# Performance work log

Hardware: AMD Instinct MI355X
Metric: run time of the kernel (lower is better)

Reference implementation:

```python
import jax, jax.numpy as jnp
import numpy as np


def _aggregate(xyz, node, features, k):
    # xyz: [B,3,N], node: [B,3,M], features: [B,C,N] -> [B,C,M]
    # squared euclidean distances via expansion (same math as (x-n)^2 sum)
    d = (jnp.sum(xyz ** 2, axis=1)[:, :, None]
         + jnp.sum(node ** 2, axis=1)[:, None, :]
         - 2.0 * jnp.einsum('bdn,bdm->bnm', xyz, node))  # [B,N,M]
    # k smallest over N for each of M nodes (order irrelevant: max-pool after)
    _, nn_idx = jax.lax.top_k(-jnp.transpose(d, (0, 2, 1)), k)  # [B,M,k]
    # gather C-channel features at neighbor indices -> [B,C,M,k]
    g = jnp.take_along_axis(features[:, :, None, :], nn_idx[:, None, :, :], axis=3)
    return jnp.max(g, axis=3)  # [B,C,M]


def setup_inputs() -> dict:
    key = jax.random.key(0)
    k1, k2, k3, k4 = jax.random.split(key, 4)
    B, N, C = 4, 16384, 128
    return {
        'input_coords': jax.random.normal(k1, (B, 3, N), dtype=jnp.float32),
        'input_feats': jax.random.normal(k2, (B, C, N), dtype=jnp.float32),
        'W': jax.random.normal(k3, (C, C), dtype=jnp.float32) * 0.05,
        'b': jax.random.normal(k4, (C,), dtype=jnp.float32) * 0.05,
        'num_sample': 2048,
        'num_agg': 16,
    }


def reference(input_coords, input_feats, W, b, num_sample, num_agg):
    # Dropout in eval mode -> identity. proj = 1x1 Conv1d == per-point linear.
    Z = input_feats  # [B,C,N]
    proj = jax.nn.relu(jnp.einsum('oc,bcn->bon', W, Z) + b[None, :, None])
    vector = jnp.max(proj, axis=-1, keepdims=True)  # [B,C,1]
    weights = jnp.sum(input_feats * vector, axis=1)  # [B,N]
    scores = jax.nn.sigmoid(weights)
    values, idx = jax.lax.top_k(scores, num_sample)  # [B,M] each, sorted desc
    pool_coords_static = jnp.take_along_axis(input_coords, idx[:, None, :], axis=2)  # [B,3,M]
    pool_feats_static = jnp.take_along_axis(input_feats, idx[:, None, :], axis=2)    # [B,C,M]
    v = values[:, None, :]  # [B,1,M]
    pool_feats = pool_feats_static * v
    pool_coords = pool_coords_static * v
    agg_feats = _aggregate(input_coords, pool_coords_static, input_feats, num_agg)  # [B,C,M]
    pool_feats = jnp.concatenate([pool_feats, agg_feats], axis=1)  # [B,2C,M]
    return (pool_coords_static, pool_coords, pool_feats)
```

## Files before the change

kernel.cpp:

```cpp
#include <hip/hip_runtime.h>
#include <hip/hip_bf16.h>
#include <stdint.h>

#define BB 4
#define NN 16384
#define CC 128
#define MM 2048
#define KNN 16
#define QCAPG 512
#define EPS 1e-3f

typedef unsigned int u32;
typedef unsigned short u16;
typedef unsigned long long u64;

#define OFF_FEATT   0ull
#define OFF_PTS4    33554432ull
#define OFF_WT      37748736ull
#define OFF_KEYS    37814272ull
#define OFF_VEC     38338560ull
#define OFF_IDX     38340608ull
#define OFF_VAL     38373376ull
#define OFF_TMP1    38406144ull
#define OFF_TMP2    38668288ull
#define OFF_QCNT    38799360ull
#define OFF_Q       38832128ull

__device__ __forceinline__ float np_dist(float4 p, float4 nd) {
#pragma clang fp contract(off)
    float dot = ((p.x * nd.x) + (p.y * nd.y)) + (p.z * nd.z);
    float d = (p.w + nd.w) - 2.0f * dot;
    return d;
}

__device__ __forceinline__ float sfast(float4 p, float4 nd) {
    float dot = fmaf(p.x, nd.x, fmaf(p.y, nd.y, p.z * nd.z));
    return fmaf(-2.0f, dot, p.w);
}

__device__ __forceinline__ u32 mono_bits(float d) {
    u32 u = __float_as_uint(d);
    u ^= ((u32)(((int)u) >> 31)) | 0x80000000u;
    return u;
}

__device__ __forceinline__ float kth16(float v, int l) {
    float sv = v;
#pragma unroll
    for (int k = 2; k <= 64; k <<= 1) {
#pragma unroll
        for (int j = k >> 1; j > 0; j >>= 1) {
            float pv = __shfl_xor(sv, j);
            bool up = ((l & k) == 0);
            bool tmin = (((l & j) == 0) == up);
            float mn = fminf(sv, pv), mx = fmaxf(sv, pv);
            sv = tmin ? mn : mx;
        }
    }
    return __shfl(sv, 15);
}

__global__ void k_prep(const float* __restrict__ coords, const float* __restrict__ W,
                       float4* __restrict__ pts4, float* __restrict__ WT,
                       u32* __restrict__ vecU, u32* __restrict__ qcnt) {
    int g = blockIdx.x * 256 + threadIdx.x;
    if (g < BB * NN) {
        int b = g >> 14, n = g & (NN - 1);
        const float* cb = coords + (size_t)b * 3 * NN;
        float x = cb[n], y = cb[NN + n], z = cb[2 * NN + n];
        float w;
        {
#pragma clang fp contract(off)
            w = ((x * x) + (y * y)) + (z * z);
        }
        pts4[g] = make_float4(x, y, z, w);
    } else if (g < BB * NN + CC * CC) {
        int i = g - BB * NN;
        int o = i >> 7, c = i & 127;
        WT[c * CC + o] = W[i];
    } else if (g < BB * NN + CC * CC + BB * CC) {
        vecU[g - BB * NN - CC * CC] = 0u;
    } else if (g < BB * NN + CC * CC + BB * CC + BB * MM) {
        qcnt[g - BB * NN - CC * CC - BB * CC] = 0u;
    }
}

__global__ void k_transpose(const float* __restrict__ feats, float* __restrict__ feat_t) {
    __shared__ float t[64][65];
    int bx = blockIdx.x;
    int b = bx >> 9; int rem = bx & 511; int nb = rem >> 1; int cb2 = rem & 1;
    int n0 = nb * 64, c0 = cb2 * 64;
    int l = threadIdx.x & 63, r0 = threadIdx.x >> 6;
    const float* fb = feats + (size_t)b * CC * NN;
#pragma unroll
    for (int p = 0; p < 16; ++p) {
        int r = r0 + p * 4;
        t[r][l] = fb[(size_t)(c0 + r) * NN + n0 + l];
    }
    __syncthreads();
    float* ob = feat_t + (size_t)b * NN * CC;
#pragma unroll
    for (int p = 0; p < 16; ++p) {
        int r = r0 + p * 4;
        ob[(size_t)(n0 + r) * CC + c0 + l] = t[l][r];
    }
}

__global__ __launch_bounds__(256, 4) void k_vec(const float* __restrict__ feats,
        const float* __restrict__ WT, const float* __restrict__ bias, u32* __restrict__ vecU) {
    __shared__ float Wl[CC * 64];
    int bx = blockIdx.x;
    int oh = bx & 1;
    int ntile = (bx >> 1) & 63;
    int b = bx >> 7;
    int n0 = ntile * 256;
    int tid = threadIdx.x, l = tid & 63;
    int w = __builtin_amdgcn_readfirstlane(tid >> 6);
    for (int i = tid; i < CC * 64; i += 256) {
        int c = i >> 6, op = i & 63;
        Wl[i] = WT[c * CC + oh * 64 + op];
    }
    __syncthreads();
    int o0 = w * 16;
    const float* zb = feats + (size_t)b * CC * NN + n0 + 4 * l;
    float bo[16];
#pragma unroll
    for (int oi = 0; oi < 16; ++oi) bo[oi] = bias[oh * 64 + o0 + oi];
    float acc0[16], acc1[16], acc2[16], acc3[16];
#pragma unroll
    for (int oi = 0; oi < 16; ++oi) { acc0[oi] = bo[oi]; acc1[oi] = bo[oi]; acc2[oi] = bo[oi]; acc3[oi] = bo[oi]; }
    float4 zpre = *(const float4*)zb;
#pragma unroll 2
    for (int c = 0; c < CC; ++c) {
        float4 z = zpre;
        if (c + 1 < CC) zpre = *(const float4*)(zb + (size_t)(c + 1) * NN);
        const float* wr = Wl + c * 64 + o0;
        float4 w0 = *(const float4*)(wr);
        float4 w1 = *(const float4*)(wr + 4);
        float4 w2 = *(const float4*)(wr + 8);
        float4 w3 = *(const float4*)(wr + 12);
        float wv[16] = {w0.x, w0.y, w0.z, w0.w, w1.x, w1.y, w1.z, w1.w,
                        w2.x, w2.y, w2.z, w2.w, w3.x, w3.y, w3.z, w3.w};
#pragma unroll
        for (int oi = 0; oi < 16; ++oi) {
            acc0[oi] = fmaf(wv[oi], z.x, acc0[oi]);
            acc1[oi] = fmaf(wv[oi], z.y, acc1[oi]);
            acc2[oi] = fmaf(wv[oi], z.z, acc2[oi]);
            acc3[oi] = fmaf(wv[oi], z.w, acc3[oi]);
        }
    }
#pragma unroll
    for (int oi = 0; oi < 16; ++oi) {
        float r0 = acc0[oi] > 0.0f ? acc0[oi] : 0.0f;
        float r1 = acc1[oi] > 0.0f ? acc1[oi] : 0.0f;
        float r2 = acc2[oi] > 0.0f ? acc2[oi] : 0.0f;
        float r3 = acc3[oi] > 0.0f ? acc3[oi] : 0.0f;
        float rv = fmaxf(fmaxf(r0, r1), fmaxf(r2, r3));
#pragma unroll
        for (int s = 32; s; s >>= 1) rv = fmaxf(rv, __shfl_xor(rv, s));
        if (l == 0) atomicMax(vecU + b * CC + oh * 64 + o0 + oi, __float_as_uint(rv));
    }
}

__global__ void k_scores(const float* __restrict__ feats, const float* __restrict__ vecF,
                         u64* __restrict__ keys) {
    int i = blockIdx.x * 256 + threadIdx.x;
    int b = i >> 14, n = i & (NN - 1);
    const float* fb = feats + (size_t)b * CC * NN + n;
    const float* vb = vecF + b * CC;
    float wsum = 0.f;
#pragma unroll 8
    for (int c = 0; c < CC; ++c) wsum = fmaf(fb[(size_t)c * NN], vb[c], wsum);
    float s = 1.0f / (1.0f + expf(-wsum));
    u32 mono = __float_as_uint(s);
    keys[i] = ((u64)mono << 32) | (u64)(0xFFFFFFFFu - (u32)n);
}

__global__ __launch_bounds__(1024) void k_sortchunk(u64* __restrict__ keys) {
    __shared__ u64 sk[2048];
    int b = blockIdx.x >> 3, c = blockIdx.x & 7;
    int tid = threadIdx.x;
    u64* src = keys + (size_t)b * NN + c * 2048;
    sk[tid] = src[tid];
    sk[tid + 1024] = src[tid + 1024];
    for (int size = 2; size <= 2048; size <<= 1) {
        for (int stride = size >> 1; stride > 0; stride >>= 1) {
            __syncthreads();
            int t = tid;
            int i = (t << 1) - (t & (stride - 1));
            int j = i + stride;
            u64 a = sk[i], cc = sk[j];
            bool up = ((i & size) == 0);
            if ((a < cc) == up) { sk[i] = cc; sk[j] = a; }
        }
    }
    __syncthreads();
    src[tid] = sk[tid];
    src[tid + 1024] = sk[tid + 1024];
}

__global__ __launch_bounds__(512) void k_mergetop(const u64* __restrict__ in,
        u64* __restrict__ outp, int lg ) {
    __shared__ u64 mk[4096];
    int b = blockIdx.x >> lg, pr = blockIdx.x & ((1 << lg) - 1);
    int tid = threadIdx.x;
    const u64* s0 = in + ((size_t)((b << lg) + pr) * 2) * 2048;
    const u64* s1 = s0 + 2048;
    for (int t = tid; t < 2048; t += 512) { mk[t] = s0[t]; mk[2048 + t] = s1[2047 - t]; }
    __syncthreads();
    for (int t = tid; t < 2048; t += 512) {
        u64 a = mk[t], c = mk[t + 2048];
        if (a < c) { mk[t] = c; mk[t + 2048] = a; }
    }
    for (int stride = 1024; stride > 0; stride >>= 1) {
        __syncthreads();
        for (int t = tid; t < 1024; t += 512) {
            int i = (t << 1) - (t & (stride - 1));
            int j = i + stride;
            u64 a = mk[i], c = mk[j];
            if (a < c) { mk[i] = c; mk[j] = a; }
        }
    }
    __syncthreads();
    u64* dst = outp + (size_t)((b << lg) + pr) * 2048;
    for (int t = tid; t < 2048; t += 512) dst[t] = mk[t];
}

__global__ __launch_bounds__(512) void k_mergefinal(const u64* __restrict__ in,
        u32* __restrict__ idxA, float* __restrict__ valA) {
    __shared__ u64 mk[4096];
    int b = blockIdx.x, tid = threadIdx.x;
    const u64* s0 = in + (size_t)(b * 2) * 2048;
    const u64* s1 = s0 + 2048;
    for (int t = tid; t < 2048; t += 512) { mk[t] = s0[t]; mk[2048 + t] = s1[2047 - t]; }
    __syncthreads();
    for (int t = tid; t < 2048; t += 512) {
        u64 a = mk[t], c = mk[t + 2048];
        if (a < c) { mk[t] = c; mk[t + 2048] = a; }
    }
    for (int stride = 1024; stride > 0; stride >>= 1) {
        __syncthreads();
        for (int t = tid; t < 1024; t += 512) {
            int i = (t << 1) - (t & (stride - 1));
            int j = i + stride;
            u64 a = mk[i], c = mk[j];
            if (a < c) { mk[i] = c; mk[j] = a; }
        }
    }
    __syncthreads();
    for (int t = tid; t < 2048; t += 512) {
        u64 k = mk[t];
        idxA[b * MM + t] = 0xFFFFFFFFu - (u32)(k & 0xFFFFFFFFull);
        valA[b * MM + t] = __uint_as_float((u32)(k >> 32));
    }
}

__global__ void k_gather(const float4* __restrict__ pts4, const float* __restrict__ feat_t,
        const u32* __restrict__ idxA, const float* __restrict__ valA, float* __restrict__ out) {
    int g = blockIdx.x * 256 + threadIdx.x;
    int b = g >> 11, i = g & (MM - 1);
    u32 n = idxA[g];
    float v = valA[g];
    float4 p = pts4[(b << 14) + (int)n];
    float* o0 = out + (size_t)b * 3 * MM + i;
    o0[0] = p.x; o0[MM] = p.y; o0[2 * MM] = p.z;
    float* o1 = o0 + 24576;
    o1[0] = p.x * v; o1[MM] = p.y * v; o1[2 * MM] = p.z * v;
    const float4* ft = (const float4*)(feat_t + ((size_t)(b << 14) + n) * CC);
    float* o2 = out + 49152 + ((size_t)b * 256) * MM + i;
#pragma unroll 8
    for (int q = 0; q < 32; ++q) {
        float4 f = ft[q];
        o2[(size_t)(4 * q + 0) * MM] = f.x * v;
        o2[(size_t)(4 * q + 1) * MM] = f.y * v;
        o2[(size_t)(4 * q + 2) * MM] = f.z * v;
        o2[(size_t)(4 * q + 3) * MM] = f.w * v;
    }
}

__device__ __forceinline__ void emit_q(u32* __restrict__ qcnt, u32* __restrict__ q,
        int gn, u64 bal, bool pred, int n, int l) {
    int cnt = (int)__popcll(bal);
    u32 base = 0;
    if (l == 0) base = atomicAdd(qcnt + gn, (u32)cnt);
    base = (u32)__shfl((int)base, 0);
    if (pred) {
        int off = (int)__popcll(bal & ((1ull << l) - 1ull));
        u32 slot = base + (u32)off;
        if (slot < QCAPG) q[(size_t)gn * QCAPG + slot] = (u32)n;
    }
}

__global__ __launch_bounds__(256) void k_knnS(const float4* __restrict__ pts4,
        const u32* __restrict__ idxA, u32* __restrict__ qcnt, u32* __restrict__ q) {
    __shared__ float4 ptsS[1024];
    __shared__ float4 nodeS[8];
    int bx = blockIdx.x;
    int b = bx >> 9;
    int idx = bx & 511;
    int ng = idx >> 1;
    int half = idx & 1;
    int tid = threadIdx.x, l = tid & 63;
    int w = __builtin_amdgcn_readfirstlane(tid >> 6);
    const float4* pb = pts4 + (b << 14);
    if (tid < 8) nodeS[tid] = pb[idxA[b * MM + ng * 8 + tid]];
#pragma unroll
    for (int j = 0; j < 4; ++j) ptsS[tid + 256 * j] = pb[tid + 256 * j];
    __syncthreads();
    float4 nd0 = nodeS[w * 2 + 0];
    float4 nd1 = nodeS[w * 2 + 1];
    float lm0 = 3.0e38f, lm1 = 3.0e38f;
#pragma unroll 4
    for (int j = 0; j < 16; ++j) {
        float4 p = ptsS[l + 64 * j];
        lm0 = fminf(lm0, sfast(p, nd0));
        lm1 = fminf(lm1, sfast(p, nd1));
    }
    __syncthreads();
#pragma unroll
    for (int j = 0; j < 4; ++j) ptsS[tid + 256 * j] = pb[1024 + tid + 256 * j];
    __syncthreads();
#pragma unroll 4
    for (int j = 0; j < 16; ++j) {
        float4 p = ptsS[l + 64 * j];
        lm0 = fminf(lm0, sfast(p, nd0));
        lm1 = fminf(lm1, sfast(p, nd1));
    }
    float T0 = kth16(lm0, l) + 2.0f * EPS;
    float T1 = kth16(lm1, l) + 2.0f * EPS;
    int gn0 = (b << 11) + ng * 8 + w * 2;
    for (int ch = half * 8; ch < half * 8 + 8; ++ch) {
        __syncthreads();
#pragma unroll
        for (int j = 0; j < 4; ++j) ptsS[tid + 256 * j] = pb[ch * 1024 + tid + 256 * j];
        __syncthreads();
        for (int j = 0; j < 16; ++j) {
            float4 p = ptsS[l + 64 * j];
            int n = ch * 1024 + l + 64 * j;
            float dt0 = fmaf(p.x, nd0.x, fmaf(p.y, nd0.y, p.z * nd0.z));
            float s0 = fmaf(-2.0f, dt0, p.w);
            float dt1 = fmaf(p.x, nd1.x, fmaf(p.y, nd1.y, p.z * nd1.z));
            float s1 = fmaf(-2.0f, dt1, p.w);
            bool p0 = (s0 <= T0);
            bool p1 = (s1 <= T1);
            u64 bal0 = __ballot(p0);
            if (bal0) emit_q(qcnt, q, gn0, bal0, p0, n, l);
            u64 bal1 = __ballot(p1);
            if (bal1) emit_q(qcnt, q, gn0 + 1, bal1, p1, n, l);
        }
    }
}

__global__ __launch_bounds__(256) void k_knnM(const float4* __restrict__ pts4,
        const float* __restrict__ feat_t, const u32* __restrict__ idxA,
        const u32* __restrict__ qcnt, const u32* __restrict__ q, float* __restrict__ out) {
    int w = __builtin_amdgcn_readfirstlane(threadIdx.x >> 6);
    int g = blockIdx.x * 4 + w;
    int b = g >> 11, m = g & (MM - 1);
    int l = threadIdx.x & 63;
    const float4* pb = pts4 + (b << 14);
    float4 nd = pb[idxA[g]];
    int cnt = (int)qcnt[g];
    if (cnt > QCAPG) cnt = QCAPG;
    const u32* qq = q + (size_t)g * QCAPG;
    u64 regk[QCAPG / 64];
#pragma unroll
    for (int s = 0; s < QCAPG / 64; ++s) {
        u64 kk = ~0ull;
        if ((s << 6) < cnt) {
            int pos = (s << 6) + l;
            if (pos < cnt) {
                u32 n = qq[pos];
                float d = np_dist(pb[n], nd);
                kk = ((u64)mono_bits(d) << 32) | (u64)n;
            }
        }
        regk[s] = kk;
    }
    float mx0 = -3.0e38f, mx1 = -3.0e38f;
    for (int it = 0; it < KNN; ++it) {
        u64 mykey = ~0ull;
#pragma unroll
        for (int s = 0; s < QCAPG / 64; ++s)
            if ((s << 6) < cnt) mykey = regk[s] < mykey ? regk[s] : mykey;
        u64 r = mykey;
#pragma unroll
        for (int j = 32; j > 0; j >>= 1) {
            u64 o = __shfl_xor(r, j);
            r = o < r ? o : r;
        }
#pragma unroll
        for (int s = 0; s < QCAPG / 64; ++s)
            if ((s << 6) < cnt) { if (regk[s] == r) regk[s] = ~0ull; }
        if (r != ~0ull) {
            u32 nj = (u32)(r & 0xFFFFFFFFull);
            const float2 f = *(const float2*)(feat_t + ((size_t)(b << 14) + nj) * CC + (l << 1));
            mx0 = fmaxf(mx0, f.x);
            mx1 = fmaxf(mx1, f.y);
        }
    }
    size_t ob = 49152 + ((size_t)(b * 256 + 128 + 2 * l)) * MM + m;
    out[ob] = mx0;
    out[ob + MM] = mx1;
}

extern "C" void kernel_launch(void* const* d_in, const int* in_sizes, int n_in,
                              void* d_out, int out_size, void* d_ws, size_t ws_size,
                              hipStream_t stream) {
    const float* coords = (const float*)d_in[0];
    const float* feats  = (const float*)d_in[1];
    const float* W      = (const float*)d_in[2];
    const float* bias   = (const float*)d_in[3];
    char* ws = (char*)d_ws;
    float*  feat_t = (float*)(ws + OFF_FEATT);
    float4* pts4   = (float4*)(ws + OFF_PTS4);
    float*  WT     = (float*)(ws + OFF_WT);
    u64*    keys   = (u64*)(ws + OFF_KEYS);
    u32*    vecU   = (u32*)(ws + OFF_VEC);
    u32*    idxA   = (u32*)(ws + OFF_IDX);
    float*  valA   = (float*)(ws + OFF_VAL);
    u64*    tmp1   = (u64*)(ws + OFF_TMP1);
    u64*    tmp2   = (u64*)(ws + OFF_TMP2);
    u32*    qcnt   = (u32*)(ws + OFF_QCNT);
    u32*    q      = (u32*)(ws + OFF_Q);
    float*  out    = (float*)d_out;

    int prepN = BB * NN + CC * CC + BB * CC + BB * MM;
    k_prep     <<<(prepN + 255) / 256, 256, 0, stream>>>(coords, W, pts4, WT, vecU, qcnt);
    k_vec      <<<512, 256, 0, stream>>>(feats, WT, bias, vecU);
    k_transpose<<<BB * (NN / 64) * (CC / 64), 256, 0, stream>>>(feats, feat_t);
    k_scores   <<<BB * NN / 256, 256, 0, stream>>>(feats, (const float*)vecU, keys);
    k_sortchunk<<<BB * 8, 1024, 0, stream>>>(keys);
    k_mergetop <<<BB * 4, 512, 0, stream>>>(keys, tmp1, 2);
    k_mergetop <<<BB * 2, 512, 0, stream>>>(tmp1, tmp2, 1);
    k_mergefinal<<<BB, 512, 0, stream>>>(tmp2, idxA, valA);
    k_gather   <<<BB * MM / 256, 256, 0, stream>>>(pts4, feat_t, idxA, valA, out);
    k_knnS     <<<2048, 256, 0, stream>>>(pts4, idxA, qcnt, q);
    k_knnM     <<<BB * MM / 4, 256, 0, stream>>>(pts4, feat_t, idxA, qcnt, q, out);
}
```

Measured before the change: 277.0 us.

## Split KNN threshold into separate kernel and transpose candidate scan to point-major tiles

Moves the per-node k-th distance threshold estimate, taken from the first 2048 points, into its own kernel that writes a threshold array. The scan kernel now gives each thread one point and loops over 256 nodes held in shared memory, with each node's threshold packed into the w component. Before, each wave kept two nodes in registers and streamed points through shared memory. The change removes the duplicated threshold work that both halves of the old split repeated and cuts shared-memory traffic and barriers. In exchange it adds a kernel launch and gives up the dual-node interleaving. The ballot, atomic and emit logic now runs once per node per wave, which may serialize on atomics.

```diff
diff --git a/kernel.cpp b/kernel.cpp
--- a/kernel.cpp
+++ b/kernel.cpp
@@ -25,6 +25,7 @@
 #define OFF_TMP2    38668288ull
 #define OFF_QCNT    38799360ull
 #define OFF_Q       38832128ull
+#define OFF_T       55609344ull
 
 __device__ __forceinline__ float np_dist(float4 p, float4 nd) {
 #pragma clang fp contract(off)
@@ -278,75 +279,58 @@
     }
 }
 
-__device__ __forceinline__ void emit_q(u32* __restrict__ qcnt, u32* __restrict__ q,
-        int gn, u64 bal, bool pred, int n, int l) {
-    int cnt = (int)__popcll(bal);
-    u32 base = 0;
-    if (l == 0) base = atomicAdd(qcnt + gn, (u32)cnt);
-    base = (u32)__shfl((int)base, 0);
-    if (pred) {
-        int off = (int)__popcll(bal & ((1ull << l) - 1ull));
-        u32 slot = base + (u32)off;
-        if (slot < QCAPG) q[(size_t)gn * QCAPG + slot] = (u32)n;
-    }
+__global__ __launch_bounds__(256) void k_knnT(const float4* __restrict__ pts4,
+        const u32* __restrict__ idxA, float* __restrict__ Tarr) {
+    int w = __builtin_amdgcn_readfirstlane(threadIdx.x >> 6);
+    int g = blockIdx.x * 4 + w;
+    int b = g >> 11;
+    int l = threadIdx.x & 63;
+    const float4* pb = pts4 + (b << 14);
+    float4 nd = pb[idxA[g]];
+    float lm = 3.0e38f;
+#pragma unroll 8
+    for (int j = 0; j < 32; ++j) lm = fminf(lm, sfast(pb[l + 64 * j], nd));
+    float T16 = kth16(lm, l);
+    if (l == 0) Tarr[g] = T16 + 2.0f * EPS;
 }
 
 __global__ __launch_bounds__(256) void k_knnS(const float4* __restrict__ pts4,
-        const u32* __restrict__ idxA, u32* __restrict__ qcnt, u32* __restrict__ q) {
-    __shared__ float4 ptsS[1024];
-    __shared__ float4 nodeS[8];
+        const u32* __restrict__ idxA, const float* __restrict__ Tarr,
+        u32* __restrict__ qcnt, u32* __restrict__ q) {
+    __shared__ float4 nodeS[256];
     int bx = blockIdx.x;
     int b = bx >> 9;
-    int idx = bx & 511;
-    int ng = idx >> 1;
-    int half = idx & 1;
+    int rem = bx & 511;
+    int tile = rem >> 3;
+    int nc = rem & 7;
     int tid = threadIdx.x, l = tid & 63;
     int w = __builtin_amdgcn_readfirstlane(tid >> 6);
     const float4* pb = pts4 + (b << 14);
-    if (tid < 8) nodeS[tid] = pb[idxA[b * MM + ng * 8 + tid]];
-#pragma unroll
-    for (int j = 0; j < 4; ++j) ptsS[tid + 256 * j] = pb[tid + 256 * j];
-    __syncthreads();
-    float4 nd0 = nodeS[w * 2 + 0];
-    float4 nd1 = nodeS[w * 2 + 1];
-    float lm0 = 3.0e38f, lm1 = 3.0e38f;
+    int gnb = (b << 11) + nc * 256;
+    {
+        float4 nd = pb[idxA[gnb + tid]];
+        nodeS[tid] = make_float4(nd.x, nd.y, nd.z, Tarr[gnb + tid]);
+    }
+    __syncthreads();
+    int n = tile * 256 + w * 64 + l;
+    float4 p = pb[n];
 #pragma unroll 4
-    for (int j = 0; j < 16; ++j) {
-        float4 p = ptsS[l + 64 * j];
-        lm0 = fminf(lm0, sfast(p, nd0));
-        lm1 = fminf(lm1, sfast(p, nd1));
-    }
-    __syncthreads();
-#pragma unroll
-    for (int j = 0; j < 4; ++j) ptsS[tid + 256 * j] = pb[1024 + tid + 256 * j];
-    __syncthreads();
-#pragma unroll 4
-    for (int j = 0; j < 16; ++j) {
-        float4 p = ptsS[l + 64 * j];
-        lm0 = fminf(lm0, sfast(p, nd0));
-        lm1 = fminf(lm1, sfast(p, nd1));
-    }
-    float T0 = kth16(lm0, l) + 2.0f * EPS;
-    float T1 = kth16(lm1, l) + 2.0f * EPS;
-    int gn0 = (b << 11) + ng * 8 + w * 2;
-    for (int ch = half * 8; ch < half * 8 + 8; ++ch) {
-        __syncthreads();
-#pragma unroll
-        for (int j = 0; j < 4; ++j) ptsS[tid + 256 * j] = pb[ch * 1024 + tid + 256 * j];
-        __syncthreads();
-        for (int j = 0; j < 16; ++j) {
-            float4 p = ptsS[l + 64 * j];
-            int n = ch * 1024 + l + 64 * j;
-            float dt0 = fmaf(p.x, nd0.x, fmaf(p.y, nd0.y, p.z * nd0.z));
-            float s0 = fmaf(-2.0f, dt0, p.w);
-            float dt1 = fmaf(p.x, nd1.x, fmaf(p.y, nd1.y, p.z * nd1.z));
-            float s1 = fmaf(-2.0f, dt1, p.w);
-            bool p0 = (s0 <= T0);
-            bool p1 = (s1 <= T1);
-            u64 bal0 = __ballot(p0);
-            if (bal0) emit_q(qcnt, q, gn0, bal0, p0, n, l);
-            u64 bal1 = __ballot(p1);
-            if (bal1) emit_q(qcnt, q, gn0 + 1, bal1, p1, n, l);
+    for (int k = 0; k < 256; ++k) {
+        float4 nt = nodeS[k];
+        float dt = fmaf(p.x, nt.x, fmaf(p.y, nt.y, p.z * nt.z));
+        float s = fmaf(-2.0f, dt, p.w);
+        bool pred = (s <= nt.w);
+        u64 bal = __ballot(pred);
+        if (bal) {
+            int cnt = (int)__popcll(bal);
+            u32 base = 0;
+            if (l == 0) base = atomicAdd(qcnt + gnb + k, (u32)cnt);
+            base = (u32)__shfl((int)base, 0);
+            if (pred) {
+                int off = (int)__popcll(bal & ((1ull << l) - 1ull));
+                u32 slot = base + (u32)off;
+                if (slot < QCAPG) q[(size_t)(gnb + k) * QCAPG + slot] = (u32)n;
+            }
         }
     }
 }
@@ -423,6 +407,7 @@
     u64*    tmp2   = (u64*)(ws + OFF_TMP2);
     u32*    qcnt   = (u32*)(ws + OFF_QCNT);
     u32*    q      = (u32*)(ws + OFF_Q);
+    float*  Tarr   = (float*)(ws + OFF_T);
     float*  out    = (float*)d_out;
 
     int prepN = BB * NN + CC * CC + BB * CC + BB * MM;
@@ -435,6 +420,7 @@
     k_mergetop <<<BB * 2, 512, 0, stream>>>(tmp1, tmp2, 1);
     k_mergefinal<<<BB, 512, 0, stream>>>(tmp2, idxA, valA);
     k_gather   <<<BB * MM / 256, 256, 0, stream>>>(pts4, feat_t, idxA, valA, out);
-    k_knnS     <<<2048, 256, 0, stream>>>(pts4, idxA, qcnt, q);
+    k_knnT     <<<BB * MM / 4, 256, 0, stream>>>(pts4, idxA, Tarr);
+    k_knnS     <<<2048, 256, 0, stream>>>(pts4, idxA, Tarr, qcnt, q);
     k_knnM     <<<BB * MM / 4, 256, 0, stream>>>(pts4, feat_t, idxA, qcnt, q, out);
 }
```

Result: slower. 514.1 us (+85.6%).
